# Kernel optimization log

Hardware: AMD Instinct MI355X
Metric: run time of the kernel (lower is better)

The kernel has to match this reference:

```python
import jax, jax.numpy as jnp
import numpy as np

# Correlation hyperparameters (from init_kwargs; PWC-Net / LCCNet config)
PAD = 4          # pad_size
K = 1            # kernel_size (kernel radius = 0, so no window box-sum needed)
MD = 4           # max_displacement
S1 = 1           # stride1 (output stride)
S2 = 1           # stride2 (displacement stride)
MULT = 1         # corr_multiply


def setup_inputs() -> dict:
    key = jax.random.key(0)
    k1, k2 = jax.random.split(key)
    input1 = jax.random.normal(k1, (8, 128, 128, 256), dtype=jnp.float32)
    input2 = jax.random.normal(k2, (8, 128, 128, 256), dtype=jnp.float32)
    return {"input1": input1, "input2": input2}


def reference(input1, input2):
    """FlowNetC-style windowed cross-correlation cost volume.

    input1, input2: [B, C, H, W] float32.
    Returns [B, D*D, topH, topW] with D = 2*(MD//S2)+1 (here 9 -> 81 channels).
    Matches correlation_cuda: pads both inputs by PAD, correlates input1 at
    each output location against input2 shifted by every displacement in the
    grid, normalized by K*K*C.
    """
    B, C, H, W = input1.shape
    kr = (K - 1) // 2                 # kernel radius (0 for K=1)
    border = MD + kr
    p1 = jnp.pad(input1, ((0, 0), (0, 0), (PAD, PAD), (PAD, PAD)))
    p2 = jnp.pad(input2, ((0, 0), (0, 0), (PAD, PAD), (PAD, PAD)))
    Hp, Wp = H + 2 * PAD, W + 2 * PAD
    topH = -(-(Hp - 2 * border) // S1)   # ceil div
    topW = -(-(Wp - 2 * border) // S1)
    ngr = MD // S2                       # neighborhood grid radius
    sumelems = K * K * C

    # Reference (center) patch grid: [B, C, topH, topW]
    a = p1[:, :,
           border:border + (topH - 1) * S1 + 1:S1,
           border:border + (topW - 1) * S1 + 1:S1]

    outs = []
    for dy in range(-ngr, ngr + 1):       # small fixed displacement set (9x9)
        for dx in range(-ngr, ngr + 1):
            oy, ox = dy * S2, dx * S2
            b = p2[:, :,
                   border + oy:border + oy + (topH - 1) * S1 + 1:S1,
                   border + ox:border + ox + (topW - 1) * S1 + 1:S1]
            outs.append(jnp.einsum('bchw,bchw->bhw', a, b))
    out = jnp.stack(outs, axis=1) * (MULT / sumelems)
    return out
```

## Files before the change

kernel.cpp:

```cpp
#include <hip/hip_runtime.h>


#define NB 8
#define NC 128
#define NH 128
#define NW 256
#define ND 9
#define CH 32768
#define SCALE (1.0f / 128.0f)

__global__ __launch_bounds__(256, 4) void corr_kernel(
    const float* __restrict__ in1, const float* __restrict__ in2,
    float* __restrict__ out)
{
    const int bid = blockIdx.x;
    const int id  = ((bid & 7) * 144 + (bid >> 3)) * 4 + (threadIdx.x >> 6);
    const int g   = threadIdx.x & 63;

    const int dyi  = id % ND;
    const int rest = id / ND;
    const int hp   = rest & 63;
    const int b    = rest >> 6;

    const int r  = g >> 5;
    const int L  = g & 31;
    const int w0 = L << 3;
    const int h  = (hp << 1) + r;
    const int hh = h + dyi - 4;
    const bool valid = ((unsigned)hh < (unsigned)NH);
    const int hhc = valid ? hh : 0;

    const float* aq = in1 + (size_t)(b * NC * NH + h)   * NW + w0;
    const float* bq = in2 + (size_t)(b * NC * NH + hhc) * NW + w0;

    float acc[8][ND];
#pragma unroll
    for (int p = 0; p < 8; ++p)
#pragma unroll
        for (int d = 0; d < ND; ++d) acc[p][d] = 0.f;

    float4 A0 = *(const float4*)(aq);
    float4 A1 = *(const float4*)(aq + 4);
    float4 B1 = *(const float4*)(bq);
    float4 B2 = *(const float4*)(bq + 4);

#pragma unroll 2
    for (int c = 0; c < NC - 1; ++c) {
        const float e0x = __shfl(B2.x, g - 1);
        const float e0y = __shfl(B2.y, g - 1);
        const float e0z = __shfl(B2.z, g - 1);
        const float e0w = __shfl(B2.w, g - 1);
        const float e3x = __shfl(B1.x, g + 1);
        const float e3y = __shfl(B1.y, g + 1);
        const float e3z = __shfl(B1.z, g + 1);
        const float e3w = __shfl(B1.w, g + 1);

        const float a_[8]  = {A0.x, A0.y, A0.z, A0.w, A1.x, A1.y, A1.z, A1.w};
        const float bw[16] = {e0x,  e0y,  e0z,  e0w,
                              B1.x, B1.y, B1.z, B1.w,
                              B2.x, B2.y, B2.z, B2.w,
                              e3x,  e3y,  e3z,  e3w};

        aq += CH; bq += CH;
        A0 = *(const float4*)(aq);
        A1 = *(const float4*)(aq + 4);
        B1 = *(const float4*)(bq);
        B2 = *(const float4*)(bq + 4);

#pragma unroll
        for (int p = 0; p < 8; ++p)
#pragma unroll
            for (int d = 0; d < ND; ++d)
                acc[p][d] += a_[p] * bw[p + d];
    }
    {
        const float e0x = __shfl(B2.x, g - 1);
        const float e0y = __shfl(B2.y, g - 1);
        const float e0z = __shfl(B2.z, g - 1);
        const float e0w = __shfl(B2.w, g - 1);
        const float e3x = __shfl(B1.x, g + 1);
        const float e3y = __shfl(B1.y, g + 1);
        const float e3z = __shfl(B1.z, g + 1);
        const float e3w = __shfl(B1.w, g + 1);

        const float a_[8]  = {A0.x, A0.y, A0.z, A0.w, A1.x, A1.y, A1.z, A1.w};
        const float bw[16] = {e0x,  e0y,  e0z,  e0w,
                              B1.x, B1.y, B1.z, B1.w,
                              B2.x, B2.y, B2.z, B2.w,
                              e3x,  e3y,  e3z,  e3w};
#pragma unroll
        for (int p = 0; p < 8; ++p)
#pragma unroll
            for (int d = 0; d < ND; ++d)
                acc[p][d] += a_[p] * bw[p + d];
    }

    float* outp = out + ((size_t)(b * (ND * ND) + dyi * ND) * NH + h) * NW + w0;
#pragma unroll
    for (int d = 0; d < ND; ++d) {
        float v[8];
#pragma unroll
        for (int p = 0; p < 8; ++p) {
            const bool kill = (!valid) ||
                              (L == 0  && (p + d) < 4) ||
                              (L == 31 && (p + d) > 11);
            v[p] = kill ? 0.0f : acc[p][d] * SCALE;
        }
        float4 lo = {v[0], v[1], v[2], v[3]};
        float4 hi = {v[4], v[5], v[6], v[7]};
        *(float4*)(outp + (size_t)d * CH)     = lo;
        *(float4*)(outp + (size_t)d * CH + 4) = hi;
    }
}

extern "C" void kernel_launch(void* const* d_in, const int* in_sizes, int n_in,
                              void* d_out, int out_size, void* d_ws, size_t ws_size,
                              hipStream_t stream) {
    const float* in1 = (const float*)d_in[0];
    const float* in2 = (const float*)d_in[1];
    float* out = (float*)d_out;
    corr_kernel<<<dim3(1152), dim3(256), 0, stream>>>(in1, in2, out);
}
```

Before: 434.3 us.

## Give each thread 4 columns and load neighbor halos directly instead of shuffling

Each wavefront now covers one full 256-wide row, with each lane handling 4 columns instead of 8 across two rows. The cross-lane shuffles for the neighbor halo are replaced by extra overlapping float4 global loads, so each lane loads 3 float4s of input2 per channel. The channel loop now double-buffers even and odd channels to prefetch deeper, and the grid size doubles. This trades shuffle work and register pressure for more redundant memory loads, which should mostly hit cache, and more blocks.

```diff
diff --git a/kernel.cpp b/kernel.cpp
--- a/kernel.cpp
+++ b/kernel.cpp
@@ -14,82 +14,98 @@
     float* __restrict__ out)
 {
     const int bid = blockIdx.x;
-    const int id  = ((bid & 7) * 144 + (bid >> 3)) * 4 + (threadIdx.x >> 6);
+    const int sid = (bid & 7) * 288 + (bid >> 3);
+    const int id  = sid * 4 + (threadIdx.x >> 6);
     const int g   = threadIdx.x & 63;
 
     const int dyi  = id % ND;
     const int rest = id / ND;
-    const int hp   = rest & 63;
-    const int b    = rest >> 6;
+    const int h    = rest & 127;
+    const int b    = rest >> 7;
 
-    const int r  = g >> 5;
-    const int L  = g & 31;
-    const int w0 = L << 3;
-    const int h  = (hp << 1) + r;
+    const int w0 = g << 2;
     const int hh = h + dyi - 4;
     const bool valid = ((unsigned)hh < (unsigned)NH);
     const int hhc = valid ? hh : 0;
 
-    const float* aq = in1 + (size_t)(b * NC * NH + h)   * NW + w0;
-    const float* bq = in2 + (size_t)(b * NC * NH + hhc) * NW + w0;
+    const float* __restrict__ pa = in1 + (size_t)(b * NC * NH + h)   * NW;
+    const float* __restrict__ pb = in2 + (size_t)(b * NC * NH + hhc) * NW;
 
-    float acc[8][ND];
+    int oa  = w0;
+    int ob0 = (g == 0)  ? 0  : (w0 - 4);
+    int ob1 = w0;
+    int ob2 = (g == 63) ? w0 : (w0 + 4);
+
+    float acc[4][ND];
 #pragma unroll
-    for (int p = 0; p < 8; ++p)
+    for (int p = 0; p < 4; ++p)
 #pragma unroll
         for (int d = 0; d < ND; ++d) acc[p][d] = 0.f;
 
-    float4 A0 = *(const float4*)(aq);
-    float4 A1 = *(const float4*)(aq + 4);
-    float4 B1 = *(const float4*)(bq);
-    float4 B2 = *(const float4*)(bq + 4);
+    float4 A_e = *(const float4*)(pa + oa);
+    float4 P_e = *(const float4*)(pb + ob0);
+    float4 Q_e = *(const float4*)(pb + ob1);
+    float4 R_e = *(const float4*)(pb + ob2);
+    oa += CH; ob0 += CH; ob1 += CH; ob2 += CH;
+    float4 A_o = *(const float4*)(pa + oa);
+    float4 P_o = *(const float4*)(pb + ob0);
+    float4 Q_o = *(const float4*)(pb + ob1);
+    float4 R_o = *(const float4*)(pb + ob2);
+    oa += CH; ob0 += CH; ob1 += CH; ob2 += CH;
 
-#pragma unroll 2
-    for (int c = 0; c < NC - 1; ++c) {
-        const float e0x = __shfl(B2.x, g - 1);
-        const float e0y = __shfl(B2.y, g - 1);
-        const float e0z = __shfl(B2.z, g - 1);
-        const float e0w = __shfl(B2.w, g - 1);
-        const float e3x = __shfl(B1.x, g + 1);
-        const float e3y = __shfl(B1.y, g + 1);
-        const float e3z = __shfl(B1.z, g + 1);
-        const float e3w = __shfl(B1.w, g + 1);
-
-        const float a_[8]  = {A0.x, A0.y, A0.z, A0.w, A1.x, A1.y, A1.z, A1.w};
-        const float bw[16] = {e0x,  e0y,  e0z,  e0w,
-                              B1.x, B1.y, B1.z, B1.w,
-                              B2.x, B2.y, B2.z, B2.w,
-                              e3x,  e3y,  e3z,  e3w};
-
-        aq += CH; bq += CH;
-        A0 = *(const float4*)(aq);
-        A1 = *(const float4*)(aq + 4);
-        B1 = *(const float4*)(bq);
-        B2 = *(const float4*)(bq + 4);
-
+#pragma unroll 1
+    for (int c = 0; c < NC - 2; c += 2) {
+        {
+            const float a_[4]  = {A_e.x, A_e.y, A_e.z, A_e.w};
+            const float bw[12] = {P_e.x, P_e.y, P_e.z, P_e.w,
+                                  Q_e.x, Q_e.y, Q_e.z, Q_e.w,
+                                  R_e.x, R_e.y, R_e.z, R_e.w};
+            A_e = *(const float4*)(pa + oa);
+            P_e = *(const float4*)(pb + ob0);
+            Q_e = *(const float4*)(pb + ob1);
+            R_e = *(const float4*)(pb + ob2);
+            oa += CH; ob0 += CH; ob1 += CH; ob2 += CH;
 #pragma unroll
-        for (int p = 0; p < 8; ++p)
+            for (int p = 0; p < 4; ++p)
+#pragma unroll
+                for (int d = 0; d < ND; ++d)
+                    acc[p][d] += a_[p] * bw[p + d];
+        }
+        {
+            const float a_[4]  = {A_o.x, A_o.y, A_o.z, A_o.w};
+            const float bw[12] = {P_o.x, P_o.y, P_o.z, P_o.w,
+                                  Q_o.x, Q_o.y, Q_o.z, Q_o.w,
+                                  R_o.x, R_o.y, R_o.z, R_o.w};
+            A_o = *(const float4*)(pa + oa);
+            P_o = *(const float4*)(pb + ob0);
+            Q_o = *(const float4*)(pb + ob1);
+            R_o = *(const float4*)(pb + ob2);
+            oa += CH; ob0 += CH; ob1 += CH; ob2 += CH;
+#pragma unroll
+            for (int p = 0; p < 4; ++p)
+#pragma unroll
+                for (int d = 0; d < ND; ++d)
+                    acc[p][d] += a_[p] * bw[p + d];
+        }
+    }
+    {
+        const float a_[4]  = {A_e.x, A_e.y, A_e.z, A_e.w};
+        const float bw[12] = {P_e.x, P_e.y, P_e.z, P_e.w,
+                              Q_e.x, Q_e.y, Q_e.z, Q_e.w,
+                              R_e.x, R_e.y, R_e.z, R_e.w};
+#pragma unroll
+        for (int p = 0; p < 4; ++p)
 #pragma unroll
             for (int d = 0; d < ND; ++d)
                 acc[p][d] += a_[p] * bw[p + d];
     }
     {
-        const float e0x = __shfl(B2.x, g - 1);
-        const float e0y = __shfl(B2.y, g - 1);
-        const float e0z = __shfl(B2.z, g - 1);
-        const float e0w = __shfl(B2.w, g - 1);
-        const float e3x = __shfl(B1.x, g + 1);
-        const float e3y = __shfl(B1.y, g + 1);
-        const float e3z = __shfl(B1.z, g + 1);
-        const float e3w = __shfl(B1.w, g + 1);
-
-        const float a_[8]  = {A0.x, A0.y, A0.z, A0.w, A1.x, A1.y, A1.z, A1.w};
-        const float bw[16] = {e0x,  e0y,  e0z,  e0w,
-                              B1.x, B1.y, B1.z, B1.w,
-                              B2.x, B2.y, B2.z, B2.w,
-                              e3x,  e3y,  e3z,  e3w};
+        const float a_[4]  = {A_o.x, A_o.y, A_o.z, A_o.w};
+        const float bw[12] = {P_o.x, P_o.y, P_o.z, P_o.w,
+                              Q_o.x, Q_o.y, Q_o.z, Q_o.w,
+                              R_o.x, R_o.y, R_o.z, R_o.w};
 #pragma unroll
-        for (int p = 0; p < 8; ++p)
+        for (int p = 0; p < 4; ++p)
 #pragma unroll
             for (int d = 0; d < ND; ++d)
                 acc[p][d] += a_[p] * bw[p + d];
@@ -98,18 +114,16 @@
     float* outp = out + ((size_t)(b * (ND * ND) + dyi * ND) * NH + h) * NW + w0;
 #pragma unroll
     for (int d = 0; d < ND; ++d) {
-        float v[8];
+        float v[4];
 #pragma unroll
-        for (int p = 0; p < 8; ++p) {
+        for (int p = 0; p < 4; ++p) {
             const bool kill = (!valid) ||
-                              (L == 0  && (p + d) < 4) ||
-                              (L == 31 && (p + d) > 11);
+                              (g == 0  && (p + d) < 4) ||
+                              (g == 63 && (p + d) > 7);
             v[p] = kill ? 0.0f : acc[p][d] * SCALE;
         }
-        float4 lo = {v[0], v[1], v[2], v[3]};
-        float4 hi = {v[4], v[5], v[6], v[7]};
-        *(float4*)(outp + (size_t)d * CH)     = lo;
-        *(float4*)(outp + (size_t)d * CH + 4) = hi;
+        float4 o4 = {v[0], v[1], v[2], v[3]};
+        *(float4*)(outp + (size_t)d * CH) = o4;
     }
 }
 
@@ -119,5 +133,5 @@
     const float* in1 = (const float*)d_in[0];
     const float* in2 = (const float*)d_in[1];
     float* out = (float*)d_out;
-    corr_kernel<<<dim3(1152), dim3(256), 0, stream>>>(in1, in2, out);
+    corr_kernel<<<dim3(2304), dim3(256), 0, stream>>>(in1, in2, out);
 }
```

New measurement: 438.5 us. Within noise of the previous version (+1.0%).

## Share input rows across dy waves via double-buffered LDS with direct global-to-LDS loads

Applied to the files above, without the earlier changes.

Each block now covers a pair of output rows and half the width for all 9 dy displacements, one wave per dy. Per channel, the needed input2 rows and the input1 rows are staged into double-buffered LDS using the global_load_lds intrinsic. This removes the redundant global reads of input1 and overlapping input2 rows that the old per-dy waves each issued, and replaces cross-lane shuffles with LDS reads. In exchange it adds a __syncthreads every channel, halves the per-thread tile to 4 pixels, and runs 576-thread blocks, which may limit occupancy and latency hiding.

```diff
diff --git a/kernel.cpp b/kernel.cpp
--- a/kernel.cpp
+++ b/kernel.cpp
@@ -1,115 +1,117 @@
 #include <hip/hip_runtime.h>
 
 
-#define NB 8
 #define NC 128
 #define NH 128
 #define NW 256
 #define ND 9
 #define CH 32768
 #define SCALE (1.0f / 128.0f)
+#define BUFSZ 2816
 
-__global__ __launch_bounds__(256, 4) void corr_kernel(
+__device__ __forceinline__ void gl_lds16(const float* gp, float* lp) {
+    __builtin_amdgcn_global_load_lds(
+        (const __attribute__((address_space(1))) void*)gp,
+        (__attribute__((address_space(3))) void*)lp, 16, 0, 0);
+}
+
+__global__ __launch_bounds__(576) void corr_kernel(
     const float* __restrict__ in1, const float* __restrict__ in2,
     float* __restrict__ out)
 {
+    __shared__ float lds[2][BUFSZ];
+
     const int bid = blockIdx.x;
-    const int id  = ((bid & 7) * 144 + (bid >> 3)) * 4 + (threadIdx.x >> 6);
+    const int sid = (bid & 7) * 128 + (bid >> 3);
+    const int wh  = sid & 1;
+    const int hp  = (sid >> 1) & 63;
+    const int b   = sid >> 7;
+
+    const int wv  = threadIdx.x >> 6;
     const int g   = threadIdx.x & 63;
+    const int r   = g >> 5;
+    const int L   = g & 31;
 
-    const int dyi  = id % ND;
-    const int rest = id / ND;
-    const int hp   = rest & 63;
-    const int b    = rest >> 6;
+    const int h0    = hp << 1;
+    const int wbase = wh << 7;
+    const int wl    = L << 2;
 
-    const int r  = g >> 5;
-    const int L  = g & 31;
-    const int w0 = L << 3;
-    const int h  = (hp << 1) + r;
-    const int hh = h + dyi - 4;
-    const bool valid = ((unsigned)hh < (unsigned)NH);
-    const int hhc = valid ? hh : 0;
+    const int row2 = min(max(h0 - 4 + wv, 0), NH - 1);
+    const int lf2  = min(max(wbase - 4 + (g << 2), 0), NW - 4);
+    const float* s2 = in2 + (size_t)(b * NC * NH + row2) * NW + lf2;
 
-    const float* aq = in1 + (size_t)(b * NC * NH + h)   * NW + w0;
-    const float* bq = in2 + (size_t)(b * NC * NH + hhc) * NW + w0;
+    const int row9 = min(h0 + 5, NH - 1);
+    const float* s9 = in2 + (size_t)(b * NC * NH + row9) * NW + lf2;
 
-    float acc[8][ND];
+    const float* s1 = in1 + (size_t)(b * NC * NH + h0 + r) * NW + wbase + wl;
+
+    const int aoff = r * 128 + wl;
+    const int boff = 256 + (r + wv) * 256 + wl;
+
+    float acc[4][ND];
 #pragma unroll
-    for (int p = 0; p < 8; ++p)
+    for (int p = 0; p < 4; ++p)
 #pragma unroll
         for (int d = 0; d < ND; ++d) acc[p][d] = 0.f;
 
-    float4 A0 = *(const float4*)(aq);
-    float4 A1 = *(const float4*)(aq + 4);
-    float4 B1 = *(const float4*)(bq);
-    float4 B2 = *(const float4*)(bq + 4);
+    gl_lds16(s2, &lds[0][256 + wv * 256]); s2 += CH;
+    if (wv == 1) { gl_lds16(s9, &lds[0][256 + 9 * 256]); s9 += CH; }
+    if (wv == 0) { gl_lds16(s1, &lds[0][0]);             s1 += CH; }
+    __syncthreads();
 
-#pragma unroll 2
+#pragma unroll 1
     for (int c = 0; c < NC - 1; ++c) {
-        const float e0x = __shfl(B2.x, g - 1);
-        const float e0y = __shfl(B2.y, g - 1);
-        const float e0z = __shfl(B2.z, g - 1);
-        const float e0w = __shfl(B2.w, g - 1);
-        const float e3x = __shfl(B1.x, g + 1);
-        const float e3y = __shfl(B1.y, g + 1);
-        const float e3z = __shfl(B1.z, g + 1);
-        const float e3w = __shfl(B1.w, g + 1);
+        const int cur = c & 1, nxt = cur ^ 1;
+        gl_lds16(s2, &lds[nxt][256 + wv * 256]); s2 += CH;
+        if (wv == 1) { gl_lds16(s9, &lds[nxt][256 + 9 * 256]); s9 += CH; }
+        if (wv == 0) { gl_lds16(s1, &lds[nxt][0]);             s1 += CH; }
 
-        const float a_[8]  = {A0.x, A0.y, A0.z, A0.w, A1.x, A1.y, A1.z, A1.w};
-        const float bw[16] = {e0x,  e0y,  e0z,  e0w,
+        const float4 A  = *(const float4*)&lds[cur][aoff];
+        const float4 B0 = *(const float4*)&lds[cur][boff];
+        const float4 B1 = *(const float4*)&lds[cur][boff + 4];
+        const float4 B2 = *(const float4*)&lds[cur][boff + 8];
+        const float a_[4]  = {A.x, A.y, A.z, A.w};
+        const float bw[12] = {B0.x, B0.y, B0.z, B0.w,
                               B1.x, B1.y, B1.z, B1.w,
-                              B2.x, B2.y, B2.z, B2.w,
-                              e3x,  e3y,  e3z,  e3w};
-
-        aq += CH; bq += CH;
-        A0 = *(const float4*)(aq);
-        A1 = *(const float4*)(aq + 4);
-        B1 = *(const float4*)(bq);
-        B2 = *(const float4*)(bq + 4);
-
+                              B2.x, B2.y, B2.z, B2.w};
 #pragma unroll
-        for (int p = 0; p < 8; ++p)
+        for (int p = 0; p < 4; ++p)
 #pragma unroll
             for (int d = 0; d < ND; ++d)
                 acc[p][d] += a_[p] * bw[p + d];
+        __syncthreads();
     }
     {
-        const float e0x = __shfl(B2.x, g - 1);
-        const float e0y = __shfl(B2.y, g - 1);
-        const float e0z = __shfl(B2.z, g - 1);
-        const float e0w = __shfl(B2.w, g - 1);
-        const float e3x = __shfl(B1.x, g + 1);
-        const float e3y = __shfl(B1.y, g + 1);
-        const float e3z = __shfl(B1.z, g + 1);
-        const float e3w = __shfl(B1.w, g + 1);
-
-        const float a_[8]  = {A0.x, A0.y, A0.z, A0.w, A1.x, A1.y, A1.z, A1.w};
-        const float bw[16] = {e0x,  e0y,  e0z,  e0w,
+        const float4 A  = *(const float4*)&lds[1][aoff];
+        const float4 B0 = *(const float4*)&lds[1][boff];
+        const float4 B1 = *(const float4*)&lds[1][boff + 4];
+        const float4 B2 = *(const float4*)&lds[1][boff + 8];
+        const float a_[4]  = {A.x, A.y, A.z, A.w};
+        const float bw[12] = {B0.x, B0.y, B0.z, B0.w,
                               B1.x, B1.y, B1.z, B1.w,
-                              B2.x, B2.y, B2.z, B2.w,
-                              e3x,  e3y,  e3z,  e3w};
+                              B2.x, B2.y, B2.z, B2.w};
 #pragma unroll
-        for (int p = 0; p < 8; ++p)
+        for (int p = 0; p < 4; ++p)
 #pragma unroll
             for (int d = 0; d < ND; ++d)
                 acc[p][d] += a_[p] * bw[p + d];
     }
 
-    float* outp = out + ((size_t)(b * (ND * ND) + dyi * ND) * NH + h) * NW + w0;
+    const bool valid = ((unsigned)(h0 + r + wv - 4) < (unsigned)NH);
+    float* outp = out + ((size_t)(b * (ND * ND) + wv * ND) * NH + (h0 + r)) * NW
+                      + wbase + wl;
 #pragma unroll
     for (int d = 0; d < ND; ++d) {
-        float v[8];
+        float v[4];
 #pragma unroll
-        for (int p = 0; p < 8; ++p) {
+        for (int p = 0; p < 4; ++p) {
             const bool kill = (!valid) ||
-                              (L == 0  && (p + d) < 4) ||
-                              (L == 31 && (p + d) > 11);
+                              (wh == 0 && L == 0  && (p + d) < 4) ||
+                              (wh == 1 && L == 31 && (p + d) > 7);
             v[p] = kill ? 0.0f : acc[p][d] * SCALE;
         }
-        float4 lo = {v[0], v[1], v[2], v[3]};
-        float4 hi = {v[4], v[5], v[6], v[7]};
-        *(float4*)(outp + (size_t)d * CH)     = lo;
-        *(float4*)(outp + (size_t)d * CH + 4) = hi;
+        float4 o4 = {v[0], v[1], v[2], v[3]};
+        *(float4*)(outp + (size_t)d * CH) = o4;
     }
 }
 
@@ -119,5 +121,5 @@
     const float* in1 = (const float*)d_in[0];
     const float* in2 = (const float*)d_in[1];
     float* out = (float*)d_out;
-    corr_kernel<<<dim3(1152), dim3(256), 0, stream>>>(in1, in2, out);
+    corr_kernel<<<dim3(1024), dim3(576), 0, stream>>>(in1, in2, out);
 }
```

Result: slower. 545.2 us (+25.5%).

## Double-buffer channel loads two deep and relax launch bounds

Applied to the files above, without the earlier changes.

The channel loop now keeps two register sets of A/B vectors (even and odd channels), so each load is issued two iterations before it is used instead of one, with manual even/odd phases and a peeled tail. Launch bounds drop from 4 to 2 blocks per SM so the compiler has room for the extra registers. This aims to hide global-memory latency better per wave, at the cost of lower occupancy and higher register pressure.

```diff
diff --git a/kernel.cpp b/kernel.cpp
--- a/kernel.cpp
+++ b/kernel.cpp
@@ -1,7 +1,6 @@
 #include <hip/hip_runtime.h>
 
 
-#define NB 8
 #define NC 128
 #define NH 128
 #define NW 256
@@ -9,7 +8,7 @@
 #define CH 32768
 #define SCALE (1.0f / 128.0f)
 
-__global__ __launch_bounds__(256, 4) void corr_kernel(
+__global__ __launch_bounds__(256, 2) void corr_kernel(
     const float* __restrict__ in1, const float* __restrict__ in2,
     float* __restrict__ out)
 {
@@ -30,8 +29,9 @@
     const bool valid = ((unsigned)hh < (unsigned)NH);
     const int hhc = valid ? hh : 0;
 
-    const float* aq = in1 + (size_t)(b * NC * NH + h)   * NW + w0;
-    const float* bq = in2 + (size_t)(b * NC * NH + hhc) * NW + w0;
+    const float* __restrict__ pa = in1 + (size_t)(b * NC * NH + h)   * NW;
+    const float* __restrict__ pb = in2 + (size_t)(b * NC * NH + hhc) * NW;
+    int oa = w0;
 
     float acc[8][ND];
 #pragma unroll
@@ -39,61 +39,78 @@
 #pragma unroll
         for (int d = 0; d < ND; ++d) acc[p][d] = 0.f;
 
-    float4 A0 = *(const float4*)(aq);
-    float4 A1 = *(const float4*)(aq + 4);
-    float4 B1 = *(const float4*)(bq);
-    float4 B2 = *(const float4*)(bq + 4);
+    float4 A0e = *(const float4*)(pa + oa);
+    float4 A1e = *(const float4*)(pa + oa + 4);
+    float4 B1e = *(const float4*)(pb + oa);
+    float4 B2e = *(const float4*)(pb + oa + 4);
+    oa += CH;
+    float4 A0o = *(const float4*)(pa + oa);
+    float4 A1o = *(const float4*)(pa + oa + 4);
+    float4 B1o = *(const float4*)(pb + oa);
+    float4 B2o = *(const float4*)(pb + oa + 4);
+    oa += CH;
 
-#pragma unroll 2
-    for (int c = 0; c < NC - 1; ++c) {
-        const float e0x = __shfl(B2.x, g - 1);
-        const float e0y = __shfl(B2.y, g - 1);
-        const float e0z = __shfl(B2.z, g - 1);
-        const float e0w = __shfl(B2.w, g - 1);
-        const float e3x = __shfl(B1.x, g + 1);
-        const float e3y = __shfl(B1.y, g + 1);
-        const float e3z = __shfl(B1.z, g + 1);
-        const float e3w = __shfl(B1.w, g + 1);
+#define PHASE(S)                                                            \
+    {                                                                       \
+        const float e0x = __shfl(B2##S.x, g - 1);                           \
+        const float e0y = __shfl(B2##S.y, g - 1);                           \
+        const float e0z = __shfl(B2##S.z, g - 1);                           \
+        const float e0w = __shfl(B2##S.w, g - 1);                           \
+        const float e3x = __shfl(B1##S.x, g + 1);                           \
+        const float e3y = __shfl(B1##S.y, g + 1);                           \
+        const float e3z = __shfl(B1##S.z, g + 1);                           \
+        const float e3w = __shfl(B1##S.w, g + 1);                           \
+        const float a_[8]  = {A0##S.x, A0##S.y, A0##S.z, A0##S.w,           \
+                              A1##S.x, A1##S.y, A1##S.z, A1##S.w};          \
+        const float bw[16] = {e0x, e0y, e0z, e0w,                           \
+                              B1##S.x, B1##S.y, B1##S.z, B1##S.w,           \
+                              B2##S.x, B2##S.y, B2##S.z, B2##S.w,           \
+                              e3x, e3y, e3z, e3w};                          \
+        _Pragma("unroll")                                                   \
+        for (int p = 0; p < 8; ++p)                                         \
+            _Pragma("unroll")                                               \
+            for (int d = 0; d < ND; ++d)                                    \
+                acc[p][d] += a_[p] * bw[p + d];                             \
+        A0##S = *(const float4*)(pa + oa);                                  \
+        A1##S = *(const float4*)(pa + oa + 4);                              \
+        B1##S = *(const float4*)(pb + oa);                                  \
+        B2##S = *(const float4*)(pb + oa + 4);                              \
+        oa += CH;                                                           \
+    }
 
-        const float a_[8]  = {A0.x, A0.y, A0.z, A0.w, A1.x, A1.y, A1.z, A1.w};
-        const float bw[16] = {e0x,  e0y,  e0z,  e0w,
-                              B1.x, B1.y, B1.z, B1.w,
-                              B2.x, B2.y, B2.z, B2.w,
-                              e3x,  e3y,  e3z,  e3w};
+#define PHASE_TAIL(S)                                                       \
+    {                                                                       \
+        const float e0x = __shfl(B2##S.x, g - 1);                           \
+        const float e0y = __shfl(B2##S.y, g - 1);                           \
+        const float e0z = __shfl(B2##S.z, g - 1);                           \
+        const float e0w = __shfl(B2##S.w, g - 1);                           \
+        const float e3x = __shfl(B1##S.x, g + 1);                           \
+        const float e3y = __shfl(B1##S.y, g + 1);                           \
+        const float e3z = __shfl(B1##S.z, g + 1);                           \
+        const float e3w = __shfl(B1##S.w, g + 1);                           \
+        const float a_[8]  = {A0##S.x, A0##S.y, A0##S.z, A0##S.w,           \
+                              A1##S.x, A1##S.y, A1##S.z, A1##S.w};          \
+        const float bw[16] = {e0x, e0y, e0z, e0w,                           \
+                              B1##S.x, B1##S.y, B1##S.z, B1##S.w,           \
+                              B2##S.x, B2##S.y, B2##S.z, B2##S.w,           \
+                              e3x, e3y, e3z, e3w};                          \
+        _Pragma("unroll")                                                   \
+        for (int p = 0; p < 8; ++p)                                         \
+            _Pragma("unroll")                                               \
+            for (int d = 0; d < ND; ++d)                                    \
+                acc[p][d] += a_[p] * bw[p + d];                             \
+    }
 
-        aq += CH; bq += CH;
-        A0 = *(const float4*)(aq);
-        A1 = *(const float4*)(aq + 4);
-        B1 = *(const float4*)(bq);
-        B2 = *(const float4*)(bq + 4);
+#pragma unroll 1
+    for (int c = 0; c < 126; c += 2) {
+        PHASE(e)
+        PHASE(o)
+    }
+    PHASE_TAIL(e)
+    PHASE_TAIL(o)
 
-#pragma unroll
-        for (int p = 0; p < 8; ++p)
-#pragma unroll
-            for (int d = 0; d < ND; ++d)
-                acc[p][d] += a_[p] * bw[p + d];
-    }
-    {
-        const float e0x = __shfl(B2.x, g - 1);
-        const float e0y = __shfl(B2.y, g - 1);
-        const float e0z = __shfl(B2.z, g - 1);
-        const float e0w = __shfl(B2.w, g - 1);
-        const float e3x = __shfl(B1.x, g + 1);
-        const float e3y = __shfl(B1.y, g + 1);
-        const float e3z = __shfl(B1.z, g + 1);
-        const float e3w = __shfl(B1.w, g + 1);
-
-        const float a_[8]  = {A0.x, A0.y, A0.z, A0.w, A1.x, A1.y, A1.z, A1.w};
-        const float bw[16] = {e0x,  e0y,  e0z,  e0w,
-                              B1.x, B1.y, B1.z, B1.w,
-                              B2.x, B2.y, B2.z, B2.w,
-                              e3x,  e3y,  e3z,  e3w};
-#pragma unroll
-        for (int p = 0; p < 8; ++p)
-#pragma unroll
-            for (int d = 0; d < ND; ++d)
-                acc[p][d] += a_[p] * bw[p + d];
-    }
+#undef PHASE
+#undef PHASE_TAIL
 
     float* outp = out + ((size_t)(b * (ND * ND) + dyi * ND) * NH + h) * NW + w0;
 #pragma unroll
```

Measured after the change: 385.0 us. 11.4% less time.
